# Kernel tuning notes

Measured on AMD Instinct MI355X. Metric: run time of the kernel, lower is better.

## Reference

```python
import jax, jax.numpy as jnp
import numpy as np

N_ENT, N_CON, DIM, R, NB = 30000, 29309, 128, 12, 8
B, LC, S, E_DB, E_CON = 256, 50, 32, 300000, 200000


def setup_inputs() -> dict:
    key = jax.random.key(0)
    ks = jax.random.split(key, 32)
    f = lambda k, sh: (jax.random.normal(k, sh, jnp.float32) * 0.02)
    concept_emb = f(ks[0], (N_CON, DIM)).at[0].set(0.0)  # padding_idx=0 row zeroed
    inp = {
        'concept_mask': jax.random.randint(ks[1], (B, LC), 0, N_CON, jnp.int32),
        'seed_pad': jax.random.randint(ks[2], (B, S), 0, N_ENT, jnp.int32),
        'seed_lens': jax.random.randint(ks[3], (B,), 0, S + 1, jnp.int32),
        'db_edge_index': jax.random.randint(ks[4], (2, E_DB), 0, N_ENT, jnp.int32),
        'db_edge_type': jax.random.randint(ks[5], (E_DB,), 0, R, jnp.int32),
        'con_edge_index': jax.random.randint(ks[6], (2, E_CON), 0, N_CON, jnp.int32),
        'db_vec': jax.random.uniform(ks[7], (B, N_ENT), jnp.float32),
        'labels': jax.random.randint(ks[8], (B,), 0, N_ENT, jnp.int64),
        'rec': jax.random.uniform(ks[9], (B,), jnp.float32),
        'concept_emb': concept_emb,
        'basis': f(ks[10], (NB, N_ENT, DIM)),
        'comp': f(ks[11], (R, NB)),
        'rgcn_root': f(ks[12], (N_ENT, DIM)),
        'rgcn_bias': jnp.zeros((DIM,), jnp.float32),
        'gcn_w': f(ks[13], (DIM, DIM)),
        'gcn_b': jnp.zeros((DIM,), jnp.float32),
        'attn_a': f(ks[14], (DIM, DIM)),
        'attn_b': f(ks[15], (DIM, 1)),
        'attn_a_db': f(ks[16], (DIM, DIM)),
        'attn_b_db': f(ks[17], (DIM, 1)),
        'user_norm_w': f(ks[18], (DIM, 2 * DIM)),
        'user_norm_b': jnp.zeros((DIM,), jnp.float32),
        'gate_norm_w': f(ks[19], (1, DIM)),
        'gate_norm_b': jnp.zeros((1,), jnp.float32),
        'info_con_w': f(ks[20], (DIM, DIM)),
        'info_con_b': jnp.zeros((DIM,), jnp.float32),
        'info_out_db_b': jnp.zeros((N_ENT,), jnp.float32),
        'output_en_b': jnp.zeros((N_ENT,), jnp.float32),
    }
    return inp


def _forward(concept_mask, seed_pad, seed_lens, db_edge_index, db_edge_type,
             con_edge_index, db_vec, labels, rec, concept_emb, basis, comp,
             rgcn_root, rgcn_bias, gcn_w, gcn_b, attn_a, attn_b, attn_a_db,
             attn_b_db, user_norm_w, user_norm_b, gate_norm_w, gate_norm_b,
             info_con_w, info_con_b, info_out_db_b, output_en_b):
    NEG = jnp.float32(-1e30)
    # ---- RGCN over DBpedia graph (x=None -> per-edge row W[rel][src]) ----
    w = jnp.einsum('rb,bnd->rnd', comp, basis)            # [R, N_ent, D]
    src, dst = db_edge_index[0], db_edge_index[1]
    msg = w[db_edge_type, src]                            # [E, D]
    agg = jax.ops.segment_sum(msg, dst, num_segments=N_ENT)
    cnt = jax.ops.segment_sum(jnp.ones_like(dst, jnp.float32), dst, num_segments=N_ENT)
    db_feats = agg / jnp.maximum(cnt, 1.0)[:, None] + rgcn_root + rgcn_bias  # mean aggr + root + bias
    # ---- GCN over concept graph (symmetric norm, self-loops) ----
    xw = concept_emb @ gcn_w
    loops = jnp.arange(N_CON, dtype=con_edge_index.dtype)
    cs = jnp.concatenate([con_edge_index[0], loops])
    cd = jnp.concatenate([con_edge_index[1], loops])
    deg = jax.ops.segment_sum(jnp.ones_like(cd, jnp.float32), cd, num_segments=N_CON)
    dinv = jnp.where(deg > 0, jax.lax.rsqrt(jnp.maximum(deg, 1e-12)), 0.0)
    norm = dinv[cs] * dinv[cd]
    con_feats = jax.ops.segment_sum(norm[:, None] * xw[cs], cd, num_segments=N_CON) + gcn_b
    # ---- per-sample seed-set self-attention over db features ----
    h = db_feats[seed_pad]                                # [B, S, D]
    e = jnp.tanh(h @ attn_a_db) @ attn_b_db               # [B, S, 1]
    valid = jnp.arange(S)[None, :] < seed_lens[:, None]   # [B, S]
    a = jax.nn.softmax(jnp.where(valid[..., None], e, NEG), axis=1)
    db_user = jnp.einsum('bso,bsd->bd', a, h)             # weighted sum (o=1)
    has_seed = (seed_lens > 0)
    db_user = jnp.where(has_seed[:, None], db_user, 0.0)  # empty seed set -> zeros
    db_con_mask = has_seed.astype(jnp.float32)
    # ---- batch self-attention over gathered concept features ----
    hc = con_feats[concept_mask]                          # [B, LC, D]
    ec = jnp.tanh(hc @ attn_a) @ attn_b                   # [B, LC, 1]
    cvalid = (concept_mask != 0)
    ac = jax.nn.softmax(jnp.where(cvalid[..., None], ec, NEG), axis=1)
    con_user = jnp.einsum('blo,bld->bd', ac, hc)
    # ---- gated fusion ----
    u = jnp.concatenate([con_user, db_user], axis=-1) @ user_norm_w.T + user_norm_b
    gate = jax.nn.sigmoid(u @ gate_norm_w.T + gate_norm_b)  # [B, 1]
    user_emb = gate * db_user + (1.0 - gate) * con_user
    entity_scores = user_emb @ db_feats.T + output_en_b   # [B, N_ent]
    # ---- infomax MSE loss ----
    con_e = con_user @ info_con_w.T + info_con_b
    db_scores = con_e @ db_feats.T + info_out_db_b
    info_db_loss = jnp.mean(jnp.sum((db_scores - db_vec) ** 2, axis=-1) * db_con_mask)
    # ---- rec CE loss ----
    logp = jax.nn.log_softmax(entity_scores, axis=-1)
    ce = -jnp.take_along_axis(logp, labels[:, None].astype(jnp.int32), axis=1)[:, 0]
    rec_loss = jnp.sum(ce * rec)
    loss = rec_loss + 0.025 * info_db_loss                # pretrain=False path
    return loss, entity_scores, rec_loss


def reference(concept_mask, seed_pad, seed_lens, db_edge_index, db_edge_type,
              con_edge_index, db_vec, labels, rec, concept_emb, basis, comp,
              rgcn_root, rgcn_bias, gcn_w, gcn_b, attn_a, attn_b, attn_a_db,
              attn_b_db, user_norm_w, user_norm_b, gate_norm_w, gate_norm_b,
              info_con_w, info_con_b, info_out_db_b, output_en_b):
    return _forward(concept_mask, seed_pad, seed_lens, db_edge_index, db_edge_type,
                    con_edge_index, db_vec, labels, rec, concept_emb, basis, comp,
                    rgcn_root, rgcn_bias, gcn_w, gcn_b, attn_a, attn_b, attn_a_db,
                    attn_b_db, user_norm_w, user_norm_b, gate_norm_w, gate_norm_b,
                    info_con_w, info_con_b, info_out_db_b, output_en_b)
```

## Files before the change

kernel.cpp:

```cpp
#include <hip/hip_runtime.h>

#define N_ENT  30000
#define N_CON  29309
#define DIM    128
#define NBASIS 8
#define NREL   12
#define BATCH  256
#define LCON   50
#define SSEED  32
#define EDB    300000
#define ECON   200000
#define NTILE  938

#define NE4      ((N_CON * DIM) / 4)
#define NB_HIST  ((EDB + ECON + 255) / 256)
#define NB_CONV  ((NE4 + 3 * (DIM * DIM / 4) + 255) / 256)
#define NB_WCOMP ((N_ENT * 32) / 256)
#define NB_PREP  (NB_HIST * 5)
#define NB_XW    ((N_CON + 127) / 128)
#define NB_RG    ((N_ENT + 3) / 4)
#define NB_GG    ((N_CON + 3) / 4)
#define NB_EDB   ((N_ENT + 31) / 32)
#define NB_ECON  ((N_CON + 31) / 32)

typedef __attribute__((ext_vector_type(8)))  short bfrag8;
typedef __attribute__((ext_vector_type(16))) float facc16;

__device__ __forceinline__ unsigned short f2bf(float f) {
    unsigned int u = __float_as_uint(f);
    u += 0x7FFFu + ((u >> 16) & 1u);
    return (unsigned short)(u >> 16);
}
__device__ __forceinline__ float bf2f(unsigned int h) {
    return __uint_as_float(h << 16);
}

__global__ __launch_bounds__(256) void prep_kernel(const int* __restrict__ db_dst,
                                                   const int* __restrict__ con_dst,
                                                   const float* __restrict__ emb,
                                                   const float* __restrict__ W,
                                                   const float* __restrict__ A_db,
                                                   const float* __restrict__ A_c,
                                                   const float* __restrict__ basis,
                                                   const float* __restrict__ comp,
                                                   int* __restrict__ cnt_e, int* __restrict__ cnt_c,
                                                   int* __restrict__ ord_db, int* __restrict__ ord_con,
                                                   unsigned short* __restrict__ emb_h,
                                                   unsigned short* __restrict__ Wt_h,
                                                   unsigned short* __restrict__ At_db_h,
                                                   unsigned short* __restrict__ At_c_h,
                                                   unsigned short* __restrict__ w_h,
                                                   int use_w) {
    __shared__ float sc[NREL * NBASIS];
    int t = threadIdx.x, bb = blockIdx.x;
    int g = bb / 5, slot = bb % 5;
    if (slot == 0) {
        int e = g * 256 + t;
        if (e < EDB) {
            ord_db[e] = atomicAdd(cnt_e + db_dst[e], 1);
        } else if (e < EDB + ECON) {
            int ee = e - EDB;
            ord_con[ee] = atomicAdd(cnt_c + con_dst[ee], 1);
        }
        return;
    }
    if (slot <= 2) {
        int cb = g * 2 + (slot - 1);
        if (cb >= NB_CONV) return;
        int i = cb * 256 + t;
        if (i < NE4) {
            float4 v = ((const float4*)emb)[i];
            unsigned int p0 = (unsigned int)f2bf(v.x) | ((unsigned int)f2bf(v.y) << 16);
            unsigned int p1 = (unsigned int)f2bf(v.z) | ((unsigned int)f2bf(v.w) << 16);
            *(uint2*)(emb_h + (size_t)i * 4) = make_uint2(p0, p1);
        } else {
            int j = i - NE4;
            if (j < 3 * (DIM * DIM) / 4) {
                int sel = j >> 12;
                int jj = j & 4095;
                const float* S = (sel == 0) ? W : ((sel == 1) ? A_db : A_c);
                unsigned short* Dst = (sel == 0) ? Wt_h : ((sel == 1) ? At_db_h : At_c_h);
                int o = jj * 4;
                int n = o >> 7, k0 = o & 127;
                unsigned int p0 = (unsigned int)f2bf(S[(k0 + 0) * DIM + n]) |
                                  ((unsigned int)f2bf(S[(k0 + 1) * DIM + n]) << 16);
                unsigned int p1 = (unsigned int)f2bf(S[(k0 + 2) * DIM + n]) |
                                  ((unsigned int)f2bf(S[(k0 + 3) * DIM + n]) << 16);
                *(uint2*)(Dst + n * DIM + k0) = make_uint2(p0, p1);
            }
        }
        return;
    }
    if (!use_w) return;
    int wb = g * 2 + (slot - 3);
    if (wb >= NB_WCOMP) return;
    if (t < NREL * NBASIS) sc[t] = comp[t];
    __syncthreads();
    int i = wb * 256 + t;
    int n = i >> 5, d4 = i & 31;
    float4 bv[NBASIS];
#pragma unroll
    for (int b = 0; b < NBASIS; ++b)
        bv[b] = ((const float4*)(basis + ((size_t)b * N_ENT + n) * DIM))[d4];
#pragma unroll
    for (int r = 0; r < NREL; ++r) {
        float4 acc = make_float4(0.f, 0.f, 0.f, 0.f);
#pragma unroll
        for (int b = 0; b < NBASIS; ++b) {
            float c = sc[r * NBASIS + b];
            acc.x += c * bv[b].x; acc.y += c * bv[b].y;
            acc.z += c * bv[b].z; acc.w += c * bv[b].w;
        }
        unsigned int p0 = (unsigned int)f2bf(acc.x) | ((unsigned int)f2bf(acc.y) << 16);
        unsigned int p1 = (unsigned int)f2bf(acc.z) | ((unsigned int)f2bf(acc.w) << 16);
        *(uint2*)(w_h + ((size_t)n * NREL + r) * DIM + d4 * 4) = make_uint2(p0, p1);
    }
}

__device__ void scan_block(const int* __restrict__ cnt, int n, int* __restrict__ rowptr) {
    __shared__ int part[1024];
    int t = threadIdx.x;
    int per = (n + 1023) / 1024;
    int s0 = t * per;
    int sum = 0;
    for (int i = 0; i < per; ++i) {
        int idx = s0 + i;
        if (idx < n) sum += cnt[idx];
    }
    part[t] = sum;
    __syncthreads();
    for (int off = 1; off < 1024; off <<= 1) {
        int v = (t >= off) ? part[t - off] : 0;
        __syncthreads();
        part[t] += v;
        __syncthreads();
    }
    int run = part[t] - sum;
    for (int i = 0; i < per; ++i) {
        int idx = s0 + i;
        if (idx < n) {
            rowptr[idx] = run;
            run += cnt[idx];
        }
    }
    if (t == 1023) rowptr[n] = part[1023];
}

__global__ __launch_bounds__(1024) void scan2_kernel(const int* __restrict__ cnt_e,
                                                     const int* __restrict__ cnt_c,
                                                     int* __restrict__ rowptr_e,
                                                     int* __restrict__ rowptr_c,
                                                     float* __restrict__ dinv,
                                                     const unsigned short* __restrict__ emb_h,
                                                     const unsigned short* __restrict__ Wt_h,
                                                     unsigned short* __restrict__ xw_h) {
    int bb = blockIdx.x;
    if (bb == 0) {
        scan_block(cnt_e, N_ENT, rowptr_e);
        return;
    }
    if (bb == 1) {
        scan_block(cnt_c, N_CON, rowptr_c);
        for (int i = threadIdx.x; i < N_CON; i += 1024)
            dinv[i] = rsqrtf((float)(cnt_c[i] + 1));
        return;
    }
    int t = threadIdx.x;
    int wave = t >> 6, lane = t & 63;
    int m0 = (bb - 2) * 128 + (wave >> 2) * 32;
    int n0 = (wave & 3) * 32;
    int am = lane & 31, ak = (lane >> 5) * 8;
    int mrow = m0 + am;
    bool mv = mrow < N_CON;
    const unsigned short* Ar = emb_h + (size_t)mrow * DIM + ak;
    const unsigned short* Br = Wt_h + (size_t)(n0 + am) * DIM + ak;
    facc16 acc;
#pragma unroll
    for (int r = 0; r < 16; ++r) acc[r] = 0.f;
#pragma unroll
    for (int s = 0; s < 8; ++s) {
        bfrag8 a;
#pragma unroll
        for (int j = 0; j < 8; ++j) a[j] = 0;
        if (mv) a = *(const bfrag8*)(Ar + s * 16);
        bfrag8 b = *(const bfrag8*)(Br + s * 16);
        acc = __builtin_amdgcn_mfma_f32_32x32x16_bf16(a, b, acc, 0, 0, 0);
    }
    int col = lane & 31;
    int g4 = (lane >> 5) * 4;
#pragma unroll
    for (int r = 0; r < 16; ++r) {
        int m = m0 + (r & 3) + ((r >> 2) << 3) + g4;
        if (m < N_CON) xw_h[(size_t)m * DIM + n0 + col] = f2bf(acc[r]);
    }
}

__global__ __launch_bounds__(256) void scatter_kernel(const int* __restrict__ db_eidx,
                                                      const int* __restrict__ db_etype,
                                                      const int* __restrict__ con_eidx,
                                                      const int* __restrict__ ord_db,
                                                      const int* __restrict__ ord_con,
                                                      const int* __restrict__ rowptr_e,
                                                      const int* __restrict__ rowptr_c,
                                                      int* __restrict__ elist_e,
                                                      int* __restrict__ elist_c) {
    int e = blockIdx.x * 256 + threadIdx.x;
    if (e < EDB) {
        int dst = db_eidx[EDB + e];
        elist_e[rowptr_e[dst] + ord_db[e]] = db_eidx[e] | (db_etype[e] << 18);
    } else if (e < EDB + ECON) {
        int ee = e - EDB;
        int dst = con_eidx[ECON + ee];
        elist_c[rowptr_c[dst] + ord_con[ee]] = con_eidx[ee];
    }
}

__global__ __launch_bounds__(256) void gathers_kernel(const int* __restrict__ rowptr_e,
                                                      const int* __restrict__ elist_e,
                                                      const unsigned short* __restrict__ w_h,
                                                      const float* __restrict__ root,
                                                      const float* __restrict__ bias,
                                                      unsigned short* __restrict__ dbf_h,
                                                      const int* __restrict__ rowptr_c,
                                                      const int* __restrict__ elist_c,
                                                      const float* __restrict__ dinv,
                                                      const unsigned short* __restrict__ xw_h,
                                                      const float* __restrict__ gcn_b,
                                                      unsigned short* __restrict__ conf_h,
                                                      int use_w) {
    int bb = blockIdx.x;
    int pair = bb >> 1;
    int lane = threadIdx.x & 63;
    if ((bb & 1) == 0) {
        if (!use_w) return;
        int wid = pair * 4 + (threadIdx.x >> 6);
        int beg = rowptr_e[wid], end = rowptr_e[wid + 1];
        float a0 = 0.f, a1 = 0.f;
        int p = beg;
        for (; p + 3 < end; p += 4) {
            int v0 = elist_e[p], v1 = elist_e[p + 1], v2 = elist_e[p + 2], v3 = elist_e[p + 3];
            unsigned int k0 = *(const unsigned int*)(w_h + ((size_t)(v0 & 0x3FFFF) * NREL + (v0 >> 18)) * DIM + lane * 2);
            unsigned int k1 = *(const unsigned int*)(w_h + ((size_t)(v1 & 0x3FFFF) * NREL + (v1 >> 18)) * DIM + lane * 2);
            unsigned int k2 = *(const unsigned int*)(w_h + ((size_t)(v2 & 0x3FFFF) * NREL + (v2 >> 18)) * DIM + lane * 2);
            unsigned int k3 = *(const unsigned int*)(w_h + ((size_t)(v3 & 0x3FFFF) * NREL + (v3 >> 18)) * DIM + lane * 2);
            a0 += bf2f(k0 & 0xFFFF) + bf2f(k1 & 0xFFFF) + bf2f(k2 & 0xFFFF) + bf2f(k3 & 0xFFFF);
            a1 += bf2f(k0 >> 16)    + bf2f(k1 >> 16)    + bf2f(k2 >> 16)    + bf2f(k3 >> 16);
        }
        for (; p < end; ++p) {
            int v = elist_e[p];
            unsigned int k = *(const unsigned int*)(w_h + ((size_t)(v & 0x3FFFF) * NREL + (v >> 18)) * DIM + lane * 2);
            a0 += bf2f(k & 0xFFFF);
            a1 += bf2f(k >> 16);
        }
        float inv = 1.f / fmaxf((float)(end - beg), 1.f);
        size_t base = (size_t)wid * DIM + lane * 2;
        float f0 = a0 * inv + root[base]     + bias[lane * 2];
        float f1 = a1 * inv + root[base + 1] + bias[lane * 2 + 1];
        *(unsigned int*)(dbf_h + base) = (unsigned int)f2bf(f0) | ((unsigned int)f2bf(f1) << 16);
        return;
    }
    if (pair >= NB_GG) return;
    int wid = pair * 4 + (threadIdx.x >> 6);
    if (wid >= N_CON) return;
    int beg = rowptr_c[wid], end = rowptr_c[wid + 1];
    float a0 = 0.f, a1 = 0.f;
    int p = beg;
    for (; p + 3 < end; p += 4) {
        int s0 = elist_c[p], s1 = elist_c[p + 1], s2 = elist_c[p + 2], s3 = elist_c[p + 3];
        float n0 = dinv[s0], n1 = dinv[s1], n2 = dinv[s2], n3 = dinv[s3];
        unsigned int k0 = *(const unsigned int*)(xw_h + (size_t)s0 * DIM + lane * 2);
        unsigned int k1 = *(const unsigned int*)(xw_h + (size_t)s1 * DIM + lane * 2);
        unsigned int k2 = *(const unsigned int*)(xw_h + (size_t)s2 * DIM + lane * 2);
        unsigned int k3 = *(const unsigned int*)(xw_h + (size_t)s3 * DIM + lane * 2);
        a0 += n0 * bf2f(k0 & 0xFFFF) + n1 * bf2f(k1 & 0xFFFF) + n2 * bf2f(k2 & 0xFFFF) + n3 * bf2f(k3 & 0xFFFF);
        a1 += n0 * bf2f(k0 >> 16)    + n1 * bf2f(k1 >> 16)    + n2 * bf2f(k2 >> 16)    + n3 * bf2f(k3 >> 16);
    }
    for (; p < end; ++p) {
        int s = elist_c[p];
        float nm = dinv[s];
        unsigned int k = *(const unsigned int*)(xw_h + (size_t)s * DIM + lane * 2);
        a0 += nm * bf2f(k & 0xFFFF);
        a1 += nm * bf2f(k >> 16);
    }
    float dv = dinv[wid];
    unsigned int ks = *(const unsigned int*)(xw_h + (size_t)wid * DIM + lane * 2);
    size_t base = (size_t)wid * DIM + lane * 2;
    float f0 = dv * a0 + dv * dv * bf2f(ks & 0xFFFF) + gcn_b[lane * 2];
    float f1 = dv * a1 + dv * dv * bf2f(ks >> 16)    + gcn_b[lane * 2 + 1];
    *(unsigned int*)(conf_h + base) = (unsigned int)f2bf(f0) | ((unsigned int)f2bf(f1) << 16);
}

__global__ __launch_bounds__(256) void rgcn_gather_basis(const int* __restrict__ rowptr,
                                                         const int* __restrict__ elist,
                                                         const float* __restrict__ basis,
                                                         const float* __restrict__ comp,
                                                         const float* __restrict__ root,
                                                         const float* __restrict__ bias,
                                                         unsigned short* __restrict__ dbf_h) {
    int wid  = blockIdx.x * 4 + (threadIdx.x >> 6);
    int lane = threadIdx.x & 63;
    if (wid >= N_ENT) return;
    int beg = rowptr[wid], end = rowptr[wid + 1];
    float a0 = 0.f, a1 = 0.f;
    for (int p = beg; p < end; ++p) {
        int v = elist[p];
        int src = v & 0x3FFFF, ty = v >> 18;
        const float* c = comp + ty * NBASIS;
#pragma unroll
        for (int b = 0; b < NBASIS; ++b) {
            const float* bp = basis + ((size_t)b * N_ENT + src) * DIM;
            a0 += c[b] * bp[lane * 2];
            a1 += c[b] * bp[lane * 2 + 1];
        }
    }
    float inv = 1.f / fmaxf((float)(end - beg), 1.f);
    size_t base = (size_t)wid * DIM + lane * 2;
    float f0 = a0 * inv + root[base]     + bias[lane * 2];
    float f1 = a1 * inv + root[base + 1] + bias[lane * 2 + 1];
    *(unsigned int*)(dbf_h + base) = (unsigned int)f2bf(f0) | ((unsigned int)f2bf(f1) << 16);
}

__device__ __forceinline__ void escore_body(const unsigned short* __restrict__ feats,
                                            const unsigned short* __restrict__ At,
                                            const float* __restrict__ v,
                                            float* __restrict__ eo,
                                            int m0, int nrow) {
    __shared__ float part[4][32];
    int t = threadIdx.x;
    int wave = t >> 6, lane = t & 63;
    int n0 = wave * 32;
    int am = lane & 31, ak = (lane >> 5) * 8;
    int mrow = m0 + am;
    bool mv = mrow < nrow;
    const unsigned short* Ar = feats + (size_t)mrow * DIM + ak;
    const unsigned short* Br = At + (size_t)(n0 + am) * DIM + ak;
    facc16 acc;
#pragma unroll
    for (int r = 0; r < 16; ++r) acc[r] = 0.f;
#pragma unroll
    for (int s = 0; s < 8; ++s) {
        bfrag8 a;
#pragma unroll
        for (int j = 0; j < 8; ++j) a[j] = 0;
        if (mv) a = *(const bfrag8*)(Ar + s * 16);
        bfrag8 b = *(const bfrag8*)(Br + s * 16);
        acc = __builtin_amdgcn_mfma_f32_32x32x16_bf16(a, b, acc, 0, 0, 0);
    }
    int col = lane & 31, g = lane >> 5;
    float vn = v[n0 + col];
#pragma unroll
    for (int r = 0; r < 16; ++r) {
        float x = tanhf(acc[r]) * vn;
#pragma unroll
        for (int off = 16; off >= 1; off >>= 1) x += __shfl_xor(x, off, 32);
        if (col == 0) {
            int row = (r & 3) + ((r >> 2) << 3) + (g << 2);
            part[wave][row] = x;
        }
    }
    __syncthreads();
    if (t < 32) {
        int m = m0 + t;
        if (m < nrow)
            eo[m] = part[0][t] + part[1][t] + part[2][t] + part[3][t];
    }
}

__global__ __launch_bounds__(256) void escores_kernel(const unsigned short* __restrict__ dbf_h,
                                                      const unsigned short* __restrict__ At_db_h,
                                                      const float* __restrict__ v_db,
                                                      float* __restrict__ e_db,
                                                      const unsigned short* __restrict__ conf_h,
                                                      const unsigned short* __restrict__ At_c_h,
                                                      const float* __restrict__ v_c,
                                                      float* __restrict__ e_con) {
    int bb = blockIdx.x;
    int pair = bb >> 1;
    if ((bb & 1) == 0) {
        if (pair >= NB_EDB) return;
        escore_body(dbf_h, At_db_h, v_db, e_db, pair * 32, N_ENT);
    } else {
        if (pair >= NB_ECON) return;
        escore_body(conf_h, At_c_h, v_c, e_con, pair * 32, N_CON);
    }
}

__global__ __launch_bounds__(256) void attn_fusion_kernel(const unsigned short* __restrict__ dbf_h,
                                                          const unsigned short* __restrict__ conf_h,
                                                          const float* __restrict__ e_db,
                                                          const float* __restrict__ e_con,
                                                          const int* __restrict__ seed_pad,
                                                          const int* __restrict__ seed_lens,
                                                          const int* __restrict__ concept_mask,
                                                          const float* __restrict__ Wu, const float* __restrict__ bu,
                                                          const float* __restrict__ gw, const float* __restrict__ gb,
                                                          const float* __restrict__ Wi, const float* __restrict__ bi,
                                                          unsigned short* __restrict__ uemb_h,
                                                          unsigned short* __restrict__ cone_h,
                                                          float* __restrict__ maskv) {
    __shared__ int srow[SSEED];
    __shared__ int crow[LCON];
    __shared__ float a_db[SSEED], a_con[LCON];
    __shared__ float du[DIM], cu[DIM], red[DIM];
    int b = blockIdx.x, t = threadIdx.x;
    int wave = t >> 6, lane = t & 63;
    int len = seed_lens[b];
    if (wave == 0) {
        float e = -1e30f;
        if (lane < SSEED) {
            int rv = seed_pad[b * SSEED + lane];
            srow[lane] = rv;
            if (lane < len) e = e_db[rv];
        }
        float m = e;
#pragma unroll
        for (int off = 16; off >= 1; off >>= 1) m = fmaxf(m, __shfl_xor(m, off, 32));
        float p = (lane < SSEED) ? __expf(e - m) : 0.f;
        float s = p;
#pragma unroll
        for (int off = 16; off >= 1; off >>= 1) s += __shfl_xor(s, off, 32);
        if (lane < SSEED) a_db[lane] = p / s;
    } else if (wave == 1) {
        float e = -1e30f;
        if (lane < LCON) {
            int rv = concept_mask[b * LCON + lane];
            crow[lane] = rv;
            if (rv != 0) e = e_con[rv];
        }
        float m = e;
#pragma unroll
        for (int off = 32; off >= 1; off >>= 1) m = fmaxf(m, __shfl_xor(m, off, 64));
        float p = (lane < LCON) ? __expf(e - m) : 0.f;
        float s = p;
#pragma unroll
        for (int off = 32; off >= 1; off >>= 1) s += __shfl_xor(s, off, 64);
        if (lane < LCON) a_con[lane] = p / s;
    }
    __syncthreads();
    if (t < DIM) {
        float acc = 0.f;
#pragma unroll
        for (int s = 0; s < SSEED; ++s)
            acc += a_db[s] * bf2f((unsigned int)dbf_h[(size_t)srow[s] * DIM + t]);
        du[t] = (len > 0) ? acc : 0.f;
    } else {
        int d = t - DIM;
        float acc = 0.f;
#pragma unroll
        for (int s = 0; s < LCON; ++s)
            acc += a_con[s] * bf2f((unsigned int)conf_h[(size_t)crow[s] * DIM + d]);
        cu[d] = acc;
    }
    __syncthreads();
    if (t < DIM) {
        float u = bu[t];
        const float* wr = Wu + t * 2 * DIM;
        for (int k = 0; k < DIM; ++k) u += cu[k] * wr[k];
        for (int k = 0; k < DIM; ++k) u += du[k] * wr[DIM + k];
        red[t] = u * gw[t];
    }
    __syncthreads();
    for (int s2 = 64; s2 > 0; s2 >>= 1) {
        if (t < s2) red[t] += red[t + s2];
        __syncthreads();
    }
    if (t < DIM) {
        float gate = 1.f / (1.f + __expf(-(red[0] + gb[0])));
        uemb_h[b * DIM + t] = f2bf(gate * du[t] + (1.f - gate) * cu[t]);
        float ce = bi[t];
        const float* wi = Wi + t * DIM;
        for (int k = 0; k < DIM; ++k) ce += cu[k] * wi[k];
        cone_h[b * DIM + t] = f2bf(ce);
    }
    if (t == 0) maskv[b] = (len > 0) ? 1.f : 0.f;
}

__global__ __launch_bounds__(256) void score_mfma(const unsigned short* __restrict__ dbf_h,
                                                  const unsigned short* __restrict__ uemb_h,
                                                  const unsigned short* __restrict__ cone_h,
                                                  const float* __restrict__ en_b,
                                                  const float* __restrict__ info_b,
                                                  const float* __restrict__ db_vec,
                                                  float* __restrict__ escore,
                                                  float* __restrict__ partM,
                                                  float* __restrict__ partS,
                                                  float* __restrict__ partQ) {
    int wave = threadIdx.x >> 6, lane = threadIdx.x & 63;
    int nt = blockIdx.x * 4 + wave;
    if (nt >= NTILE) return;
    int b0 = blockIdx.y * 32;
    int n0 = nt * 32;
    int am = lane & 31, ak = (lane >> 5) * 8;
    int nb = n0 + am;
    bool bvalid = nb < N_ENT;
    const unsigned short* Au = uemb_h + (size_t)(b0 + am) * DIM + ak;
    const unsigned short* Ac = cone_h + (size_t)(b0 + am) * DIM + ak;
    const unsigned short* Bp = dbf_h + (size_t)nb * DIM + ak;
    facc16 accE, accD;
#pragma unroll
    for (int r = 0; r < 16; ++r) { accE[r] = 0.f; accD[r] = 0.f; }
#pragma unroll
    for (int s = 0; s < 8; ++s) {
        bfrag8 au = *(const bfrag8*)(Au + s * 16);
        bfrag8 ac = *(const bfrag8*)(Ac + s * 16);
        bfrag8 bb;
#pragma unroll
        for (int j = 0; j < 8; ++j) bb[j] = 0;
        if (bvalid) bb = *(const bfrag8*)(Bp + s * 16);
        accE = __builtin_amdgcn_mfma_f32_32x32x16_bf16(au, bb, accE, 0, 0, 0);
        accD = __builtin_amdgcn_mfma_f32_32x32x16_bf16(ac, bb, accD, 0, 0, 0);
    }
    int col = lane & 31;
    int n = n0 + col;
    bool nv = n < N_ENT;
    float enb = nv ? en_b[n] : 0.f;
    float inb = nv ? info_b[n] : 0.f;
    int g4 = (lane >> 5) * 4;
#pragma unroll
    for (int r = 0; r < 16; ++r) {
        int b = b0 + (r & 3) + ((r >> 2) << 3) + g4;
        float e = accE[r] + enb;
        if (nv) escore[(size_t)b * N_ENT + n] = e;
        float ev = nv ? e : -1e30f;
        float mx = ev;
#pragma unroll
        for (int off = 16; off >= 1; off >>= 1) mx = fmaxf(mx, __shfl_xor(mx, off, 64));
        float ex = nv ? __expf(e - mx) : 0.f;
        float sm = ex;
#pragma unroll
        for (int off = 16; off >= 1; off >>= 1) sm += __shfl_xor(sm, off, 64);
        float d = nv ? (accD[r] + inb - db_vec[(size_t)b * N_ENT + n]) : 0.f;
        float q = d * d;
#pragma unroll
        for (int off = 16; off >= 1; off >>= 1) q += __shfl_xor(q, off, 64);
        if (col == 0) {
            partM[(size_t)b * NTILE + nt] = mx;
            partS[(size_t)b * NTILE + nt] = sm;
            partQ[(size_t)b * NTILE + nt] = q;
        }
    }
}

__global__ __launch_bounds__(256) void ce_final(const float* __restrict__ partM,
                                                const float* __restrict__ partS,
                                                const float* __restrict__ partQ,
                                                const float* __restrict__ escore,
                                                const int* __restrict__ labels,
                                                const float* __restrict__ rec,
                                                float* __restrict__ rloss,
                                                float* __restrict__ ssqv) {
    __shared__ float red[256], red2[256];
    int b = blockIdx.x, t = threadIdx.x;
    const float* pm = partM + (size_t)b * NTILE;
    const float* ps = partS + (size_t)b * NTILE;
    const float* pq = partQ + (size_t)b * NTILE;
    float mx = -1e30f;
    for (int i = t; i < NTILE; i += 256) mx = fmaxf(mx, pm[i]);
    red[t] = mx;
    __syncthreads();
    for (int s2 = 128; s2 > 0; s2 >>= 1) {
        if (t < s2) red[t] = fmaxf(red[t], red[t + s2]);
        __syncthreads();
    }
    float M = red[0];
    __syncthreads();
    float s = 0.f, q = 0.f;
    for (int i = t; i < NTILE; i += 256) {
        s += ps[i] * __expf(pm[i] - M);
        q += pq[i];
    }
    red[t] = s; red2[t] = q;
    __syncthreads();
    for (int s2 = 128; s2 > 0; s2 >>= 1) {
        if (t < s2) { red[t] += red[t + s2]; red2[t] += red2[t + s2]; }
        __syncthreads();
    }
    if (t == 0) {
        float lse = M + logf(red[0]);
        float ce  = -(escore[(size_t)b * N_ENT + labels[b]] - lse);
        rloss[b]  = ce * rec[b];
        ssqv[b]   = red2[0];
    }
}

__global__ __launch_bounds__(256) void final_kernel(const float* __restrict__ rloss,
                                                    const float* __restrict__ sumsq,
                                                    const float* __restrict__ maskv,
                                                    float* __restrict__ out) {
    __shared__ float r1[256], r2[256];
    int t = threadIdx.x;
    r1[t] = rloss[t];
    r2[t] = sumsq[t] * maskv[t];
    __syncthreads();
    for (int s2 = 128; s2 > 0; s2 >>= 1) {
        if (t < s2) { r1[t] += r1[t + s2]; r2[t] += r2[t + s2]; }
        __syncthreads();
    }
    if (t == 0) {
        float rec_loss = r1[0];
        float info = r2[0] / (float)BATCH;
        out[0] = rec_loss + 0.025f * info;
        out[1 + (size_t)BATCH * N_ENT] = rec_loss;
    }
}

extern "C" void kernel_launch(void* const* d_in, const int* in_sizes, int n_in,
                              void* d_out, int out_size, void* d_ws, size_t ws_size,
                              hipStream_t stream) {
    (void)in_sizes; (void)n_in; (void)out_size;
    const int*   concept_mask  = (const int*)d_in[0];
    const int*   seed_pad      = (const int*)d_in[1];
    const int*   seed_lens     = (const int*)d_in[2];
    const int*   db_eidx       = (const int*)d_in[3];
    const int*   db_etype      = (const int*)d_in[4];
    const int*   con_eidx      = (const int*)d_in[5];
    const float* db_vec        = (const float*)d_in[6];
    const int*   labels        = (const int*)d_in[7];
    const float* rec           = (const float*)d_in[8];
    const float* concept_emb   = (const float*)d_in[9];
    const float* basis         = (const float*)d_in[10];
    const float* comp          = (const float*)d_in[11];
    const float* rgcn_root     = (const float*)d_in[12];
    const float* rgcn_bias     = (const float*)d_in[13];
    const float* gcn_w         = (const float*)d_in[14];
    const float* gcn_b         = (const float*)d_in[15];
    const float* attn_a        = (const float*)d_in[16];
    const float* attn_b        = (const float*)d_in[17];
    const float* attn_a_db     = (const float*)d_in[18];
    const float* attn_b_db     = (const float*)d_in[19];
    const float* user_norm_w   = (const float*)d_in[20];
    const float* user_norm_b   = (const float*)d_in[21];
    const float* gate_norm_w   = (const float*)d_in[22];
    const float* gate_norm_b   = (const float*)d_in[23];
    const float* info_con_w    = (const float*)d_in[24];
    const float* info_con_b    = (const float*)d_in[25];
    const float* info_out_db_b = (const float*)d_in[26];
    const float* output_en_b   = (const float*)d_in[27];

    float* ws = (float*)d_ws;
    size_t off = 0;
    auto alloc = [&](size_t n) { float* p = ws + off; off += (n + 255) & ~(size_t)255; return p; };
    float* dinv   = alloc(N_CON);
    float* maskv  = alloc(BATCH);
    float* rls    = alloc(BATCH);
    float* ssqv   = alloc(BATCH);
    float* partM  = alloc((size_t)BATCH * NTILE);
    float* partS  = alloc((size_t)BATCH * NTILE);
    float* partQ  = alloc((size_t)BATCH * NTILE);
    int* cnt_e    = (int*)alloc(N_ENT + N_CON);
    int* cnt_c    = cnt_e + N_ENT;
    int* rowptr_e = (int*)alloc(N_ENT + 1);
    int* rowptr_c = (int*)alloc(N_CON + 1);
    int* ord_db   = (int*)alloc(EDB);
    int* ord_con  = (int*)alloc(ECON);
    int* elist_e  = (int*)alloc(EDB);
    int* elist_c  = (int*)alloc(ECON);
    unsigned short* dbf_h  = (unsigned short*)alloc((size_t)N_ENT * DIM / 2);
    unsigned short* conf_h = (unsigned short*)alloc((size_t)N_CON * DIM / 2 + 128);
    unsigned short* xw_h   = (unsigned short*)alloc((size_t)N_CON * DIM / 2 + 128);
    unsigned short* emb_h  = (unsigned short*)alloc((size_t)N_CON * DIM / 2 + 128);
    unsigned short* Wt_h   = (unsigned short*)alloc(DIM * DIM / 2);
    unsigned short* uemb_h = (unsigned short*)alloc(BATCH * DIM / 2);
    unsigned short* cone_h = (unsigned short*)alloc(BATCH * DIM / 2);
    float* e_db   = alloc(N_ENT);
    float* e_con  = alloc(N_CON);
    unsigned short* At_db_h = (unsigned short*)alloc(DIM * DIM / 2);
    unsigned short* At_c_h  = (unsigned short*)alloc(DIM * DIM / 2);
    size_t w_elems = ((size_t)NREL * N_ENT * DIM) / 2;
    int use_w = (off + w_elems) * sizeof(float) <= ws_size;
    unsigned short* w_h = (unsigned short*)(ws + off);

    float* out    = (float*)d_out;
    float* escore = out + 1;

    (void)hipMemsetAsync(cnt_e, 0, (N_ENT + N_CON) * sizeof(int), stream);

    prep_kernel<<<NB_PREP, 256, 0, stream>>>(
        db_eidx + EDB, con_eidx + ECON, concept_emb, gcn_w, attn_a_db, attn_a,
        basis, comp, cnt_e, cnt_c, ord_db, ord_con, emb_h, Wt_h, At_db_h, At_c_h,
        w_h, use_w);
    scan2_kernel<<<2 + NB_XW, 1024, 0, stream>>>(cnt_e, cnt_c, rowptr_e, rowptr_c, dinv,
                                                 emb_h, Wt_h, xw_h);
    scatter_kernel<<<NB_HIST, 256, 0, stream>>>(db_eidx, db_etype, con_eidx,
                                                ord_db, ord_con, rowptr_e, rowptr_c,
                                                elist_e, elist_c);
    gathers_kernel<<<NB_RG * 2, 256, 0, stream>>>(rowptr_e, elist_e, w_h, rgcn_root, rgcn_bias,
                                                  dbf_h, rowptr_c, elist_c, dinv, xw_h, gcn_b,
                                                  conf_h, use_w);
    if (!use_w) {
        rgcn_gather_basis<<<NB_RG, 256, 0, stream>>>(rowptr_e, elist_e, basis, comp,
                                                     rgcn_root, rgcn_bias, dbf_h);
    }
    escores_kernel<<<NB_EDB * 2, 256, 0, stream>>>(dbf_h, At_db_h, attn_b_db, e_db,
                                                   conf_h, At_c_h, attn_b, e_con);
    attn_fusion_kernel<<<BATCH, 256, 0, stream>>>(dbf_h, conf_h, e_db, e_con,
                                                  seed_pad, seed_lens, concept_mask,
                                                  user_norm_w, user_norm_b, gate_norm_w, gate_norm_b,
                                                  info_con_w, info_con_b, uemb_h, cone_h, maskv);
    dim3 sg((NTILE + 3) / 4, BATCH / 32);
    score_mfma<<<sg, 256, 0, stream>>>(dbf_h, uemb_h, cone_h, output_en_b, info_out_db_b, db_vec,
                                       escore, partM, partS, partQ);
    ce_final<<<BATCH, 256, 0, stream>>>(partM, partS, partQ, escore, labels, rec, rls, ssqv);
    final_kernel<<<1, 256, 0, stream>>>(rls, ssqv, maskv, out);
}
```

Baseline: 506.9 us.

## Widen gather lanes, pre-transpose fusion weights, fuse final reduction into CE kernel

The RGCN and GCN gathers now use 32 lanes per node with 8-byte bf16 loads, so each block covers 8 nodes and the gathers need fewer, wider memory transactions. User-norm and info-con weights are transposed in the prep kernel so the attention-fusion matvecs read coalesced columns. The final loss kernel is folded into ce_final using a last-block atomic counter, and score stores become nontemporal. Together these cut launch overhead and uncoalesced reads, at the cost of extra prep work and a grid-wide atomic completion pattern.

```diff
diff --git a/kernel.cpp b/kernel.cpp
--- a/kernel.cpp
+++ b/kernel.cpp
@@ -14,12 +14,13 @@
 
 #define NE4      ((N_CON * DIM) / 4)
 #define NB_HIST  ((EDB + ECON + 255) / 256)
-#define NB_CONV  ((NE4 + 3 * (DIM * DIM / 4) + 255) / 256)
+#define NB_CONV  ((NE4 + 24576 + 255) / 256)
 #define NB_WCOMP ((N_ENT * 32) / 256)
 #define NB_PREP  (NB_HIST * 5)
 #define NB_XW    ((N_CON + 127) / 128)
 #define NB_RG    ((N_ENT + 3) / 4)
-#define NB_GG    ((N_CON + 3) / 4)
+#define NB_RG8   ((N_ENT + 7) / 8)
+#define NB_GG8   ((N_CON + 7) / 8)
 #define NB_EDB   ((N_ENT + 31) / 32)
 #define NB_ECON  ((N_CON + 31) / 32)
 
@@ -33,6 +34,9 @@
 }
 __device__ __forceinline__ float bf2f(unsigned int h) {
     return __uint_as_float(h << 16);
+}
+__device__ __forceinline__ unsigned int pk(float a, float b) {
+    return (unsigned int)f2bf(a) | ((unsigned int)f2bf(b) << 16);
 }
 
 __global__ __launch_bounds__(256) void prep_kernel(const int* __restrict__ db_dst,
@@ -41,6 +45,8 @@
                                                    const float* __restrict__ W,
                                                    const float* __restrict__ A_db,
                                                    const float* __restrict__ A_c,
+                                                   const float* __restrict__ Wu,
+                                                   const float* __restrict__ Wi,
                                                    const float* __restrict__ basis,
                                                    const float* __restrict__ comp,
                                                    int* __restrict__ cnt_e, int* __restrict__ cnt_c,
@@ -49,6 +55,8 @@
                                                    unsigned short* __restrict__ Wt_h,
                                                    unsigned short* __restrict__ At_db_h,
                                                    unsigned short* __restrict__ At_c_h,
+                                                   float* __restrict__ WuT,
+                                                   float* __restrict__ WiT,
                                                    unsigned short* __restrict__ w_h,
                                                    int use_w) {
     __shared__ float sc[NREL * NBASIS];
@@ -70,24 +78,44 @@
         int i = cb * 256 + t;
         if (i < NE4) {
             float4 v = ((const float4*)emb)[i];
-            unsigned int p0 = (unsigned int)f2bf(v.x) | ((unsigned int)f2bf(v.y) << 16);
-            unsigned int p1 = (unsigned int)f2bf(v.z) | ((unsigned int)f2bf(v.w) << 16);
-            *(uint2*)(emb_h + (size_t)i * 4) = make_uint2(p0, p1);
-        } else {
-            int j = i - NE4;
-            if (j < 3 * (DIM * DIM) / 4) {
-                int sel = j >> 12;
-                int jj = j & 4095;
-                const float* S = (sel == 0) ? W : ((sel == 1) ? A_db : A_c);
-                unsigned short* Dst = (sel == 0) ? Wt_h : ((sel == 1) ? At_db_h : At_c_h);
-                int o = jj * 4;
-                int n = o >> 7, k0 = o & 127;
-                unsigned int p0 = (unsigned int)f2bf(S[(k0 + 0) * DIM + n]) |
-                                  ((unsigned int)f2bf(S[(k0 + 1) * DIM + n]) << 16);
-                unsigned int p1 = (unsigned int)f2bf(S[(k0 + 2) * DIM + n]) |
-                                  ((unsigned int)f2bf(S[(k0 + 3) * DIM + n]) << 16);
-                *(uint2*)(Dst + n * DIM + k0) = make_uint2(p0, p1);
-            }
+            *(uint2*)(emb_h + (size_t)i * 4) = make_uint2(pk(v.x, v.y), pk(v.z, v.w));
+            return;
+        }
+        int j = i - NE4;
+        if (j < 12288) {
+            int sel = j >> 12;
+            int jj = j & 4095;
+            const float* S = (sel == 0) ? W : ((sel == 1) ? A_db : A_c);
+            unsigned short* Dst = (sel == 0) ? Wt_h : ((sel == 1) ? At_db_h : At_c_h);
+            int o = jj * 4;
+            int n = o >> 7, k0 = o & 127;
+            unsigned int p0 = pk(S[(k0 + 0) * DIM + n], S[(k0 + 1) * DIM + n]);
+            unsigned int p1 = pk(S[(k0 + 2) * DIM + n], S[(k0 + 3) * DIM + n]);
+            *(uint2*)(Dst + n * DIM + k0) = make_uint2(p0, p1);
+            return;
+        }
+        int j2 = j - 12288;
+        if (j2 < 8192) {
+            int o = j2 * 4;
+            int k = o >> 7, t0 = o & 127;
+            float4 vv;
+            vv.x = Wu[(t0 + 0) * (2 * DIM) + k];
+            vv.y = Wu[(t0 + 1) * (2 * DIM) + k];
+            vv.z = Wu[(t0 + 2) * (2 * DIM) + k];
+            vv.w = Wu[(t0 + 3) * (2 * DIM) + k];
+            *(float4*)(WuT + k * DIM + t0) = vv;
+            return;
+        }
+        int j3 = j2 - 8192;
+        if (j3 < 4096) {
+            int o = j3 * 4;
+            int k = o >> 7, t0 = o & 127;
+            float4 vv;
+            vv.x = Wi[(t0 + 0) * DIM + k];
+            vv.y = Wi[(t0 + 1) * DIM + k];
+            vv.z = Wi[(t0 + 2) * DIM + k];
+            vv.w = Wi[(t0 + 3) * DIM + k];
+            *(float4*)(WiT + k * DIM + t0) = vv;
         }
         return;
     }
@@ -111,9 +139,8 @@
             acc.x += c * bv[b].x; acc.y += c * bv[b].y;
             acc.z += c * bv[b].z; acc.w += c * bv[b].w;
         }
-        unsigned int p0 = (unsigned int)f2bf(acc.x) | ((unsigned int)f2bf(acc.y) << 16);
-        unsigned int p1 = (unsigned int)f2bf(acc.z) | ((unsigned int)f2bf(acc.w) << 16);
-        *(uint2*)(w_h + ((size_t)n * NREL + r) * DIM + d4 * 4) = make_uint2(p0, p1);
+        *(uint2*)(w_h + ((size_t)n * NREL + r) * DIM + d4 * 4) =
+            make_uint2(pk(acc.x, acc.y), pk(acc.z, acc.w));
     }
 }
 
@@ -230,64 +257,79 @@
                                                       int use_w) {
     int bb = blockIdx.x;
     int pair = bb >> 1;
-    int lane = threadIdx.x & 63;
+    int half = threadIdx.x >> 5;
+    int lane = threadIdx.x & 31;
     if ((bb & 1) == 0) {
         if (!use_w) return;
-        int wid = pair * 4 + (threadIdx.x >> 6);
+        int wid = pair * 8 + half;
         int beg = rowptr_e[wid], end = rowptr_e[wid + 1];
-        float a0 = 0.f, a1 = 0.f;
+        float a0 = 0.f, a1 = 0.f, a2 = 0.f, a3 = 0.f;
         int p = beg;
         for (; p + 3 < end; p += 4) {
             int v0 = elist_e[p], v1 = elist_e[p + 1], v2 = elist_e[p + 2], v3 = elist_e[p + 3];
-            unsigned int k0 = *(const unsigned int*)(w_h + ((size_t)(v0 & 0x3FFFF) * NREL + (v0 >> 18)) * DIM + lane * 2);
-            unsigned int k1 = *(const unsigned int*)(w_h + ((size_t)(v1 & 0x3FFFF) * NREL + (v1 >> 18)) * DIM + lane * 2);
-            unsigned int k2 = *(const unsigned int*)(w_h + ((size_t)(v2 & 0x3FFFF) * NREL + (v2 >> 18)) * DIM + lane * 2);
-            unsigned int k3 = *(const unsigned int*)(w_h + ((size_t)(v3 & 0x3FFFF) * NREL + (v3 >> 18)) * DIM + lane * 2);
-            a0 += bf2f(k0 & 0xFFFF) + bf2f(k1 & 0xFFFF) + bf2f(k2 & 0xFFFF) + bf2f(k3 & 0xFFFF);
-            a1 += bf2f(k0 >> 16)    + bf2f(k1 >> 16)    + bf2f(k2 >> 16)    + bf2f(k3 >> 16);
+            uint2 k0 = *(const uint2*)(w_h + ((size_t)(v0 & 0x3FFFF) * NREL + (v0 >> 18)) * DIM + lane * 4);
+            uint2 k1 = *(const uint2*)(w_h + ((size_t)(v1 & 0x3FFFF) * NREL + (v1 >> 18)) * DIM + lane * 4);
+            uint2 k2 = *(const uint2*)(w_h + ((size_t)(v2 & 0x3FFFF) * NREL + (v2 >> 18)) * DIM + lane * 4);
+            uint2 k3 = *(const uint2*)(w_h + ((size_t)(v3 & 0x3FFFF) * NREL + (v3 >> 18)) * DIM + lane * 4);
+            a0 += bf2f(k0.x & 0xFFFF) + bf2f(k1.x & 0xFFFF) + bf2f(k2.x & 0xFFFF) + bf2f(k3.x & 0xFFFF);
+            a1 += bf2f(k0.x >> 16)    + bf2f(k1.x >> 16)    + bf2f(k2.x >> 16)    + bf2f(k3.x >> 16);
+            a2 += bf2f(k0.y & 0xFFFF) + bf2f(k1.y & 0xFFFF) + bf2f(k2.y & 0xFFFF) + bf2f(k3.y & 0xFFFF);
+            a3 += bf2f(k0.y >> 16)    + bf2f(k1.y >> 16)    + bf2f(k2.y >> 16)    + bf2f(k3.y >> 16);
         }
         for (; p < end; ++p) {
             int v = elist_e[p];
-            unsigned int k = *(const unsigned int*)(w_h + ((size_t)(v & 0x3FFFF) * NREL + (v >> 18)) * DIM + lane * 2);
-            a0 += bf2f(k & 0xFFFF);
-            a1 += bf2f(k >> 16);
+            uint2 k = *(const uint2*)(w_h + ((size_t)(v & 0x3FFFF) * NREL + (v >> 18)) * DIM + lane * 4);
+            a0 += bf2f(k.x & 0xFFFF);
+            a1 += bf2f(k.x >> 16);
+            a2 += bf2f(k.y & 0xFFFF);
+            a3 += bf2f(k.y >> 16);
         }
         float inv = 1.f / fmaxf((float)(end - beg), 1.f);
-        size_t base = (size_t)wid * DIM + lane * 2;
-        float f0 = a0 * inv + root[base]     + bias[lane * 2];
-        float f1 = a1 * inv + root[base + 1] + bias[lane * 2 + 1];
-        *(unsigned int*)(dbf_h + base) = (unsigned int)f2bf(f0) | ((unsigned int)f2bf(f1) << 16);
+        size_t base = (size_t)wid * DIM + lane * 4;
+        int d0 = lane * 4;
+        float f0 = a0 * inv + root[base]     + bias[d0];
+        float f1 = a1 * inv + root[base + 1] + bias[d0 + 1];
+        float f2 = a2 * inv + root[base + 2] + bias[d0 + 2];
+        float f3 = a3 * inv + root[base + 3] + bias[d0 + 3];
+        *(uint2*)(dbf_h + base) = make_uint2(pk(f0, f1), pk(f2, f3));
         return;
     }
-    if (pair >= NB_GG) return;
-    int wid = pair * 4 + (threadIdx.x >> 6);
+    if (pair >= NB_GG8) return;
+    int wid = pair * 8 + half;
     if (wid >= N_CON) return;
     int beg = rowptr_c[wid], end = rowptr_c[wid + 1];
-    float a0 = 0.f, a1 = 0.f;
+    float a0 = 0.f, a1 = 0.f, a2 = 0.f, a3 = 0.f;
     int p = beg;
     for (; p + 3 < end; p += 4) {
         int s0 = elist_c[p], s1 = elist_c[p + 1], s2 = elist_c[p + 2], s3 = elist_c[p + 3];
         float n0 = dinv[s0], n1 = dinv[s1], n2 = dinv[s2], n3 = dinv[s3];
-        unsigned int k0 = *(const unsigned int*)(xw_h + (size_t)s0 * DIM + lane * 2);
-        unsigned int k1 = *(const unsigned int*)(xw_h + (size_t)s1 * DIM + lane * 2);
-        unsigned int k2 = *(const unsigned int*)(xw_h + (size_t)s2 * DIM + lane * 2);
-        unsigned int k3 = *(const unsigned int*)(xw_h + (size_t)s3 * DIM + lane * 2);
-        a0 += n0 * bf2f(k0 & 0xFFFF) + n1 * bf2f(k1 & 0xFFFF) + n2 * bf2f(k2 & 0xFFFF) + n3 * bf2f(k3 & 0xFFFF);
-        a1 += n0 * bf2f(k0 >> 16)    + n1 * bf2f(k1 >> 16)    + n2 * bf2f(k2 >> 16)    + n3 * bf2f(k3 >> 16);
+        uint2 k0 = *(const uint2*)(xw_h + (size_t)s0 * DIM + lane * 4);
+        uint2 k1 = *(const uint2*)(xw_h + (size_t)s1 * DIM + lane * 4);
+        uint2 k2 = *(const uint2*)(xw_h + (size_t)s2 * DIM + lane * 4);
+        uint2 k3 = *(const uint2*)(xw_h + (size_t)s3 * DIM + lane * 4);
+        a0 += n0 * bf2f(k0.x & 0xFFFF) + n1 * bf2f(k1.x & 0xFFFF) + n2 * bf2f(k2.x & 0xFFFF) + n3 * bf2f(k3.x & 0xFFFF);
+        a1 += n0 * bf2f(k0.x >> 16)    + n1 * bf2f(k1.x >> 16)    + n2 * bf2f(k2.x >> 16)    + n3 * bf2f(k3.x >> 16);
+        a2 += n0 * bf2f(k0.y & 0xFFFF) + n1 * bf2f(k1.y & 0xFFFF) + n2 * bf2f(k2.y & 0xFFFF) + n3 * bf2f(k3.y & 0xFFFF);
+        a3 += n0 * bf2f(k0.y >> 16)    + n1 * bf2f(k1.y >> 16)    + n2 * bf2f(k2.y >> 16)    + n3 * bf2f(k3.y >> 16);
     }
     for (; p < end; ++p) {
         int s = elist_c[p];
         float nm = dinv[s];
-        unsigned int k = *(const unsigned int*)(xw_h + (size_t)s * DIM + lane * 2);
-        a0 += nm * bf2f(k & 0xFFFF);
-        a1 += nm * bf2f(k >> 16);
+        uint2 k = *(const uint2*)(xw_h + (size_t)s * DIM + lane * 4);
+        a0 += nm * bf2f(k.x & 0xFFFF);
+        a1 += nm * bf2f(k.x >> 16);
+        a2 += nm * bf2f(k.y & 0xFFFF);
+        a3 += nm * bf2f(k.y >> 16);
     }
     float dv = dinv[wid];
-    unsigned int ks = *(const unsigned int*)(xw_h + (size_t)wid * DIM + lane * 2);
-    size_t base = (size_t)wid * DIM + lane * 2;
-    float f0 = dv * a0 + dv * dv * bf2f(ks & 0xFFFF) + gcn_b[lane * 2];
-    float f1 = dv * a1 + dv * dv * bf2f(ks >> 16)    + gcn_b[lane * 2 + 1];
-    *(unsigned int*)(conf_h + base) = (unsigned int)f2bf(f0) | ((unsigned int)f2bf(f1) << 16);
+    uint2 ks = *(const uint2*)(xw_h + (size_t)wid * DIM + lane * 4);
+    size_t base = (size_t)wid * DIM + lane * 4;
+    int d0 = lane * 4;
+    float f0 = dv * a0 + dv * dv * bf2f(ks.x & 0xFFFF) + gcn_b[d0];
+    float f1 = dv * a1 + dv * dv * bf2f(ks.x >> 16)    + gcn_b[d0 + 1];
+    float f2 = dv * a2 + dv * dv * bf2f(ks.y & 0xFFFF) + gcn_b[d0 + 2];
+    float f3 = dv * a3 + dv * dv * bf2f(ks.y >> 16)    + gcn_b[d0 + 3];
+    *(uint2*)(conf_h + base) = make_uint2(pk(f0, f1), pk(f2, f3));
 }
 
 __global__ __launch_bounds__(256) void rgcn_gather_basis(const int* __restrict__ rowptr,
@@ -317,7 +359,7 @@
     size_t base = (size_t)wid * DIM + lane * 2;
     float f0 = a0 * inv + root[base]     + bias[lane * 2];
     float f1 = a1 * inv + root[base + 1] + bias[lane * 2 + 1];
-    *(unsigned int*)(dbf_h + base) = (unsigned int)f2bf(f0) | ((unsigned int)f2bf(f1) << 16);
+    *(unsigned int*)(dbf_h + base) = pk(f0, f1);
 }
 
 __device__ __forceinline__ void escore_body(const unsigned short* __restrict__ feats,
@@ -392,9 +434,9 @@
                                                           const int* __restrict__ seed_pad,
                                                           const int* __restrict__ seed_lens,
                                                           const int* __restrict__ concept_mask,
-                                                          const float* __restrict__ Wu, const float* __restrict__ bu,
+                                                          const float* __restrict__ WuT, const float* __restrict__ bu,
                                                           const float* __restrict__ gw, const float* __restrict__ gb,
-                                                          const float* __restrict__ Wi, const float* __restrict__ bi,
+                                                          const float* __restrict__ WiT, const float* __restrict__ bi,
                                                           unsigned short* __restrict__ uemb_h,
                                                           unsigned short* __restrict__ cone_h,
                                                           float* __restrict__ maskv) {
@@ -454,9 +496,8 @@
     __syncthreads();
     if (t < DIM) {
         float u = bu[t];
-        const float* wr = Wu + t * 2 * DIM;
-        for (int k = 0; k < DIM; ++k) u += cu[k] * wr[k];
-        for (int k = 0; k < DIM; ++k) u += du[k] * wr[DIM + k];
+        for (int k = 0; k < DIM; ++k) u += cu[k] * WuT[k * DIM + t];
+        for (int k = 0; k < DIM; ++k) u += du[k] * WuT[(DIM + k) * DIM + t];
         red[t] = u * gw[t];
     }
     __syncthreads();
@@ -468,8 +509,7 @@
         float gate = 1.f / (1.f + __expf(-(red[0] + gb[0])));
         uemb_h[b * DIM + t] = f2bf(gate * du[t] + (1.f - gate) * cu[t]);
         float ce = bi[t];
-        const float* wi = Wi + t * DIM;
-        for (int k = 0; k < DIM; ++k) ce += cu[k] * wi[k];
+        for (int k = 0; k < DIM; ++k) ce += cu[k] * WiT[k * DIM + t];
         cone_h[b * DIM + t] = f2bf(ce);
     }
     if (t == 0) maskv[b] = (len > 0) ? 1.f : 0.f;
@@ -520,7 +560,7 @@
     for (int r = 0; r < 16; ++r) {
         int b = b0 + (r & 3) + ((r >> 2) << 3) + g4;
         float e = accE[r] + enb;
-        if (nv) escore[(size_t)b * N_ENT + n] = e;
+        if (nv) __builtin_nontemporal_store(e, &escore[(size_t)b * N_ENT + n]);
         float ev = nv ? e : -1e30f;
         float mx = ev;
 #pragma unroll
@@ -548,8 +588,12 @@
                                                 const int* __restrict__ labels,
                                                 const float* __restrict__ rec,
                                                 float* __restrict__ rloss,
-                                                float* __restrict__ ssqv) {
+                                                float* __restrict__ ssqv,
+                                                const float* __restrict__ maskv,
+                                                float* __restrict__ out,
+                                                int* __restrict__ counter) {
     __shared__ float red[256], red2[256];
+    __shared__ int lastFlag;
     int b = blockIdx.x, t = threadIdx.x;
     const float* pm = partM + (size_t)b * NTILE;
     const float* ps = partS + (size_t)b * NTILE;
@@ -580,25 +624,23 @@
         float ce  = -(escore[(size_t)b * N_ENT + labels[b]] - lse);
         rloss[b]  = ce * rec[b];
         ssqv[b]   = red2[0];
-    }
-}
-
-__global__ __launch_bounds__(256) void final_kernel(const float* __restrict__ rloss,
-                                                    const float* __restrict__ sumsq,
-                                                    const float* __restrict__ maskv,
-                                                    float* __restrict__ out) {
-    __shared__ float r1[256], r2[256];
-    int t = threadIdx.x;
-    r1[t] = rloss[t];
-    r2[t] = sumsq[t] * maskv[t];
+        __threadfence();
+        int old = atomicAdd(counter, 1);
+        lastFlag = (old == BATCH - 1);
+    }
+    __syncthreads();
+    if (!lastFlag) return;
+    __threadfence();
+    red[t]  = rloss[t];
+    red2[t] = ssqv[t] * maskv[t];
     __syncthreads();
     for (int s2 = 128; s2 > 0; s2 >>= 1) {
-        if (t < s2) { r1[t] += r1[t + s2]; r2[t] += r2[t + s2]; }
+        if (t < s2) { red[t] += red[t + s2]; red2[t] += red2[t + s2]; }
         __syncthreads();
     }
     if (t == 0) {
-        float rec_loss = r1[0];
-        float info = r2[0] / (float)BATCH;
+        float rec_loss = red[0];
+        float info = red2[0] / (float)BATCH;
         out[0] = rec_loss + 0.025f * info;
         out[1 + (size_t)BATCH * N_ENT] = rec_loss;
     }
@@ -647,8 +689,9 @@
     float* partM  = alloc((size_t)BATCH * NTILE);
     float* partS  = alloc((size_t)BATCH * NTILE);
     float* partQ  = alloc((size_t)BATCH * NTILE);
-    int* cnt_e    = (int*)alloc(N_ENT + N_CON);
+    int* cnt_e    = (int*)alloc(N_ENT + N_CON + 64);
     int* cnt_c    = cnt_e + N_ENT;
+    int* counter  = cnt_e + N_ENT + N_CON;
     int* rowptr_e = (int*)alloc(N_ENT + 1);
     int* rowptr_c = (int*)alloc(N_CON + 1);
     int* ord_db   = (int*)alloc(EDB);
@@ -666,6 +709,8 @@
     float* e_con  = alloc(N_CON);
     unsigned short* At_db_h = (unsigned short*)alloc(DIM * DIM / 2);
     unsigned short* At_c_h  = (unsigned short*)alloc(DIM * DIM / 2);
+    float* WuT    = alloc(2 * DIM * DIM);
+    float* WiT    = alloc(DIM * DIM);
     size_t w_elems = ((size_t)NREL * N_ENT * DIM) / 2;
     int use_w = (off + w_elems) * sizeof(float) <= ws_size;
     unsigned short* w_h = (unsigned short*)(ws + off);
@@ -673,20 +718,20 @@
     float* out    = (float*)d_out;
     float* escore = out + 1;
 
-    (void)hipMemsetAsync(cnt_e, 0, (N_ENT + N_CON) * sizeof(int), stream);
+    (void)hipMemsetAsync(cnt_e, 0, (N_ENT + N_CON + 64) * sizeof(int), stream);
 
     prep_kernel<<<NB_PREP, 256, 0, stream>>>(
         db_eidx + EDB, con_eidx + ECON, concept_emb, gcn_w, attn_a_db, attn_a,
-        basis, comp, cnt_e, cnt_c, ord_db, ord_con, emb_h, Wt_h, At_db_h, At_c_h,
-        w_h, use_w);
+        user_norm_w, info_con_w, basis, comp, cnt_e, cnt_c, ord_db, ord_con,
+        emb_h, Wt_h, At_db_h, At_c_h, WuT, WiT, w_h, use_w);
     scan2_kernel<<<2 + NB_XW, 1024, 0, stream>>>(cnt_e, cnt_c, rowptr_e, rowptr_c, dinv,
                                                  emb_h, Wt_h, xw_h);
     scatter_kernel<<<NB_HIST, 256, 0, stream>>>(db_eidx, db_etype, con_eidx,
                                                 ord_db, ord_con, rowptr_e, rowptr_c,
                                                 elist_e, elist_c);
-    gathers_kernel<<<NB_RG * 2, 256, 0, stream>>>(rowptr_e, elist_e, w_h, rgcn_root, rgcn_bias,
-                                                  dbf_h, rowptr_c, elist_c, dinv, xw_h, gcn_b,
-                                                  conf_h, use_w);
+    gathers_kernel<<<NB_RG8 * 2, 256, 0, stream>>>(rowptr_e, elist_e, w_h, rgcn_root, rgcn_bias,
+                                                   dbf_h, rowptr_c, elist_c, dinv, xw_h, gcn_b,
+                                                   conf_h, use_w);
     if (!use_w) {
         rgcn_gather_basis<<<NB_RG, 256, 0, stream>>>(rowptr_e, elist_e, basis, comp,
                                                      rgcn_root, rgcn_bias, dbf_h);
@@ -695,11 +740,11 @@
                                                    conf_h, At_c_h, attn_b, e_con);
     attn_fusion_kernel<<<BATCH, 256, 0, stream>>>(dbf_h, conf_h, e_db, e_con,
                                                   seed_pad, seed_lens, concept_mask,
-                                                  user_norm_w, user_norm_b, gate_norm_w, gate_norm_b,
-                                                  info_con_w, info_con_b, uemb_h, cone_h, maskv);
+                                                  WuT, user_norm_b, gate_norm_w, gate_norm_b,
+                                                  WiT, info_con_b, uemb_h, cone_h, maskv);
     dim3 sg((NTILE + 3) / 4, BATCH / 32);
     score_mfma<<<sg, 256, 0, stream>>>(dbf_h, uemb_h, cone_h, output_en_b, info_out_db_b, db_vec,
                                        escore, partM, partS, partQ);
-    ce_final<<<BATCH, 256, 0, stream>>>(partM, partS, partQ, escore, labels, rec, rls, ssqv);
-    final_kernel<<<1, 256, 0, stream>>>(rls, ssqv, maskv, out);
-}
+    ce_final<<<BATCH, 256, 0, stream>>>(partM, partS, partQ, escore, labels, rec, rls, ssqv,
+                                        maskv, out, counter);
+}
```

Result: no change. 504.0 us (-0.6%).
